# Optimization experiments

Measured on AMD Instinct MI355X. Metric: run time of the kernel, lower is better.

The kernel has to match this reference:

```python
import jax, jax.numpy as jnp
import numpy as np

THRESHOLD = 0.9
N = 20000
K = 32
F = 64


def setup_inputs() -> dict:
    key = jax.random.key(0)
    k1, k2, k3, k4, k5 = jax.random.split(key, 5)
    features = jax.random.normal(k1, (N, F), dtype=jnp.float32)
    score = jax.random.normal(k2, (N, 1), dtype=jnp.float32)
    distances = jax.random.uniform(k3, (N, K), dtype=jnp.float32)
    # two equal segments; neighbours sampled within own segment, self at col 0
    row_splits = jnp.array([0, N // 2, N], dtype=jnp.int32)
    segN = N // 2
    local_self = (jnp.arange(N, dtype=jnp.int32) % segN)
    seg_start = (jnp.arange(N, dtype=jnp.int32) // segN) * segN
    r = jax.random.randint(k4, (N, K - 1), 0, segN - 1, dtype=jnp.int32)
    r = r + (r >= local_self[:, None]).astype(jnp.int32)  # avoid sampling self
    neigh = seg_start[:, None] + r
    nidxs = jnp.concatenate([jnp.arange(N, dtype=jnp.int32)[:, None], neigh], axis=1)
    tidxs = jax.random.randint(k5, (N, 1), 0, 50, dtype=jnp.int32)
    return {"features": features, "score": score, "distances": distances,
            "nidxs": nidxs, "row_splits": row_splits, "tidxs": tidxs}


def _lnc(features, score_logits, nidxs, row_splits):
    n, k = nidxs.shape
    score = jax.nn.sigmoid(score_logits[:, 0])  # [N]
    # hierarchy order: per row-split segment, descending score
    seg_id = jnp.searchsorted(row_splits, jnp.arange(n), side='right') - 1
    order = jnp.lexsort((-score, seg_id))

    arangeK = jnp.arange(k)

    def step(carry, p):
        ggather, sel, npg, gcount = carry
        already = ggather[p] >= 0
        high = score[p] > THRESHOLD
        m = nidxs[p]                                   # [K], m[0] == p (self)
        free = (m >= 0) & (ggather[jnp.clip(m, 0, n - 1)] < 0)
        self_only = arangeK == 0
        valid = jnp.where(high, free, self_only) & (~already) & (m >= 0)
        g = gcount
        idx_w = jnp.where(valid, m, n)                 # dummy slot n for masked writes
        ggather = ggather.at[idx_w].set(g)
        row_i = jnp.where(already, n, g)
        sel = sel.at[row_i].set(jnp.where(valid, m, -1))
        npg = npg.at[row_i].set(jnp.sum(valid.astype(jnp.int32)))
        created = (~already).astype(jnp.int32)
        return (ggather, sel, npg, gcount + created), created

    init = (jnp.full((n + 1,), -1, jnp.int32),
            jnp.full((n + 1, k), -1, jnp.int32),
            jnp.zeros((n + 1,), jnp.int32),
            jnp.int32(0))
    (ggather, sel, npg, gcount), created = jax.lax.scan(step, init, order)
    ggather, sel, npg = ggather[:n], sel[:n], npg[:n]

    # new row splits: cumulative group count at segment boundaries
    cum = jnp.cumsum(created)
    rs_new = jnp.concatenate([jnp.zeros((1,), jnp.int32),
                              cum[row_splits[1:] - 1].astype(jnp.int32)])

    # pooled features per group (rows >= gcount are padding)
    sel_c = jnp.clip(sel, 0, n - 1)
    gathered = features[sel_c]                         # [N, K, F]
    mask = (sel >= 0)[..., None]
    out_mean = jnp.sum(jnp.where(mask, gathered, 0.0), axis=1)
    out_mean = out_mean / (npg[:, None].astype(features.dtype) + 1e-6)
    out_max = jnp.max(jnp.where(mask, gathered, -1000.0), axis=1)
    out = jnp.concatenate([out_mean, out_max], axis=-1)  # [N, 2F]
    backgather = ggather[:, None]
    return out, rs_new, backgather


def reference(features, score, distances, nidxs, row_splits, tidxs):
    # distances/tidxs only feed the (disabled) loss branch; kept for signature parity
    return _lnc(features, score, nidxs, row_splits)
```

## Files before the change

kernel.cpp:

```cpp
#include <hip/hip_runtime.h>


constexpr int KN = 32;
constexpr int FD = 64;
constexpr int HOCAP = 512;
constexpr int EW = 16;
constexpr int NBB = 2048;
constexpr int NT = 256;
constexpr int NMAX = 20000;
constexpr int BSLOT = 64;

typedef unsigned long long u64;


__global__ void k0_init(const float* __restrict__ score, float* __restrict__ s,
                        int* __restrict__ grab, u64* __restrict__ hlkStage,
                        int* __restrict__ hcnt, int* __restrict__ lcnt0,
                        int* __restrict__ lcnt1, u64* __restrict__ key,
                        const int* __restrict__ row_splits, int n) {
  __shared__ int ch, cl0, cl1;
  int tid = (int)threadIdx.x, bid = (int)blockIdx.x;
  int x = bid * NT + tid;
  int lane = tid & 63;
  int half = row_splits[1];
  if (tid == 0) { ch = 0; cl0 = 0; cl1 = 0; }
  __syncthreads();
  bool hi = false, lo = false;
  u64 pk = 0;
  if (x < n) {
    float sp = 1.0f / (1.0f + expf(-score[x]));
    s[x] = sp; grab[x] = 0x7FFFFFFF;
    hi = sp > 0.9f; lo = !hi;
    unsigned sb = __float_as_uint(sp);
    pk = ((u64)(x >= half) << 63) | ((u64)(0x7FFFFFFFu - sb) << 32) | (unsigned)x;
    key[x] = lo ? (((u64)sb << 32) | (u64)(0xFFFFFFFFu - (unsigned)x)) : 0ull;
  }
  u64 bh = __ballot(hi);
  u64 b0 = __ballot(lo && x < half);
  u64 b1 = __ballot(lo && x >= half);
  int base = 0;
  if (lane == 0) {
    if (bh) base = atomicAdd(&ch, __popcll(bh));
    if (b0) atomicAdd(&cl0, __popcll(b0));
    if (b1) atomicAdd(&cl1, __popcll(b1));
  }
  base = __shfl(base, 0);
  if (hi) {
    int idx = base + __popcll(bh & ((1ull << lane) - 1ull));
    if (idx < BSLOT) hlkStage[bid * BSLOT + idx] = pk;
  }
  __syncthreads();
  if (tid == 0) {
    hcnt[bid] = (ch > BSLOT) ? BSLOT : ch;
    lcnt0[bid] = cl0; lcnt1[bid] = cl1;
  }
}

__global__ __launch_bounds__(1024, 1) void kA(
    const u64* __restrict__ hlkStage, const int* __restrict__ hcnt,
    const int* __restrict__ lcnt0, const int* __restrict__ lcnt1,
    const int* __restrict__ nidxs, const int* __restrict__ row_splits,
    int* __restrict__ nbm, int* __restrict__ fgj, int* __restrict__ fgp,
    int* __restrict__ counters, int n) {
  __shared__ unsigned short hr16[NMAX];
  __shared__ unsigned E[HOCAP * EW];
  __shared__ u64 hk[HOCAP];
  __shared__ int hol[HOCAP];
  __shared__ int fgjL[HOCAP];
  __shared__ int fgpL[HOCAP];
  __shared__ int cnts[128];
  __shared__ int pref[129];
  __shared__ int lsum[2];
  __shared__ int shg;
  int tid = (int)threadIdx.x;
  int lane = tid & 63;
  int half = row_splits[1];
  int nblk = (n + NT - 1) / NT; if (nblk > 128) nblk = 128;

  {
    unsigned* h32 = (unsigned*)hr16;
    for (int i = tid; i < NMAX / 2; i += 1024) h32[i] = 0xFFFFFFFFu;
  }
  for (int i = tid; i < HOCAP * EW; i += 1024) E[i] = 0u;
  if (tid < 128) cnts[tid] = (tid < nblk) ? hcnt[tid] : 0;
  if (tid == 0) { lsum[0] = 0; lsum[1] = 0; }
  __syncthreads();

  if (tid < 64) {
    int v0 = cnts[tid], v1 = cnts[64 + tid];
#pragma unroll
    for (int off = 1; off < 64; off <<= 1) {
      int t0 = __shfl_up(v0, off), t1 = __shfl_up(v1, off);
      if (lane >= off) { v0 += t0; v1 += t1; }
    }
    int s0 = __shfl(v0, 63);
    pref[tid + 1] = v0;
    pref[64 + tid + 1] = v1 + s0;
    if (tid == 0) pref[0] = 0;
  }
  if (tid >= 64 && tid < 192) {
    int b = tid - 64;
    if (b < nblk) { atomicAdd(&lsum[0], lcnt0[b]); atomicAdd(&lsum[1], lcnt1[b]); }
  }
  __syncthreads();
  int nh = pref[nblk]; if (nh > HOCAP) nh = HOCAP;

  for (int t = tid; t < nblk * BSLOT; t += 1024) {
    int b = t >> 6, j = t & (BSLOT - 1);
    if (j < cnts[b]) {
      int d = pref[b] + j;
      if (d < HOCAP) hk[d] = hlkStage[t];
    }
  }
  __syncthreads();

  for (int i = tid; i < nh; i += 1024) {
    u64 kp = hk[i];
    int rk = 0;
#pragma unroll 8
    for (int j = 0; j < nh; ++j) rk += (hk[j] < kp) ? 1 : 0;
    int p = (int)(unsigned)(kp & 0xFFFFFFFFu);
    hol[rk] = p; hr16[p] = (unsigned short)rk;
  }
  __syncthreads();

  {
    const int4* nsrc = (const int4*)nidxs;
    int4* ndstG = (int4*)nbm;
    int tot = nh * 8;
    for (int t = tid; t < tot; t += 1024) {
      int j = t >> 3, q4 = t & 7;
      int p = hol[j];
      int4 v = nsrc[p * 8 + q4];
      ndstG[t] = v;
      unsigned bit = 1u << (j & 31);
      unsigned widx = (unsigned)(j >> 5);
      int xs[4] = { v.x, v.y, v.z, v.w };
#pragma unroll
      for (int e = 0; e < 4; ++e) {
        unsigned r = ((unsigned)xs[e] < (unsigned)n) ? hr16[xs[e]] : 0xFFFFu;
        if (r != 0xFFFFu) atomicOr(&E[r * EW + widx], bit);
      }
    }
  }
  __syncthreads();

  if (tid < 64) {
    unsigned Fw[16];
#pragma unroll
    for (int w = 0; w < 16; ++w) Fw[w] = 0u;
    int hg = 0, h0 = 0, h1 = 0;
    u64 mask_lt = (1ull << lane) - 1ull;
#pragma unroll
    for (int c = 0; c < HOCAP / 64; ++c) {
      if (c * 64 >= nh) break;
      int j = c * 64 + lane;
      bool valid = j < nh;
      unsigned er[16];
#pragma unroll
      for (int w = 0; w < 16; ++w) er[w] = valid ? E[j * EW + w] : 0u;
      unsigned acc = 0;
#pragma unroll
      for (int w = 0; w < 16; ++w) acc |= er[w] & Fw[w];
      bool base_already = acc != 0u;
      u64 erc = ((u64)er[2 * c + 1] << 32) | er[2 * c];
      u64 fb = 0;
      for (int l = 0; l < 64; ++l) {
        bool already = base_already || ((erc & fb) != 0ull);
        bool formed = valid && !already;
        fb |= __ballot(formed && (lane == l));
      }
      Fw[2 * c]     |= (unsigned)(fb & 0xFFFFFFFFull);
      Fw[2 * c + 1] |= (unsigned)(fb >> 32);
      bool formed = (fb >> lane) & 1ull;
      int p = valid ? hol[j] : 0;
      if (formed) {
        int idx = hg + __popcll(fb & mask_lt);
        fgjL[idx] = j; fgpL[idx] = p;
      }
      h0 += __popcll(__ballot(formed && p < half));
      h1 += __popcll(__ballot(formed && p >= half));
      hg += __popcll(fb);
    }
    if (lane == 0) {
      counters[1] = hg; counters[2] = h0; counters[3] = h1; shg = hg;
    }
  }
  __syncthreads();
  int hg = shg;
  for (int i = tid; i < hg; i += 1024) { fgj[i] = fgjL[i]; fgp[i] = fgpL[i]; }
  if (tid == 0) {
    counters[0] = nh;
    counters[4] = lsum[0];
    counters[5] = lsum[1];
  }
}

__global__ void kG(const float* __restrict__ s, const int* __restrict__ nbm,
                   const int* __restrict__ fgj, int* __restrict__ grab,
                   u64* __restrict__ key, int* __restrict__ counters,
                   const int* __restrict__ row_splits, int n) {
  int t = (int)(blockIdx.x * blockDim.x + threadIdx.x);
  int lane = (int)threadIdx.x & 63;
  int half = row_splits[1];
  int hg = counters[1];
  bool gl0 = false, gl1 = false;
  if (t < hg * KN) {
    int g = t >> 5;
    int x = nbm[fgj[g] * KN + (t & 31)];
    if ((unsigned)x < (unsigned)n) {
      int old = atomicMin(&grab[x], g);
      if (old == 0x7FFFFFFF && !(s[x] > 0.9f)) {
        key[x] = 0ull;
        if (x < half) gl0 = true; else gl1 = true;
      }
    }
  }
  u64 b0 = __ballot(gl0), b1 = __ballot(gl1);
  if (lane == 0) {
    if (b0) atomicSub(&counters[4], __popcll(b0));
    if (b1) atomicSub(&counters[5], __popcll(b1));
  }
}

__global__ void kB(const int* __restrict__ row_splits, const u64* __restrict__ key,
                   const int* __restrict__ grab, const int* __restrict__ nbm,
                   const int* __restrict__ fgj, const int* __restrict__ fgp,
                   const int* __restrict__ counters, int* __restrict__ gowner,
                   unsigned* __restrict__ gmask, float* __restrict__ out,
                   int n, int rs_off) {
  int tid = (int)threadIdx.x, bid = (int)blockIdx.x;
  int gtid = bid * NT + tid;
  int lane = tid & 63;
  int half = row_splits[1];
  const int GSZ = NBB * NT;
  const int NW = GSZ >> 6;
  int wid = gtid >> 6;
  int hg = counters[1], H0 = counters[2], H1 = counters[3];
  int L0 = counters[4], L1 = counters[5];
  int bg = rs_off + 3;

  for (int x = gtid; x < n; x += GSZ) {
    int prov = grab[x];
    if (prov != 0x7FFFFFFF)
      out[bg + x] = (float)((prov < H0) ? prov : (prov + L0));
  }

  for (int tsk = wid; tsk < ((n + 7) >> 3); tsk += NW) {
    int p0 = tsk * 8;
    u64 kp[8];
#pragma unroll
    for (int i = 0; i < 8; ++i) kp[i] = (p0 + i < n) ? key[p0 + i] : 0ull;
    u64 anyk = 0;
#pragma unroll
    for (int i = 0; i < 8; ++i) anyk |= kp[i];
    if (anyk == 0ull) continue;
    int base2 = (p0 < half) ? 0 : (half >> 1);
    int npair = ((p0 < half) ? half : (n - half)) >> 1;
    const ulonglong2* key2 = (const ulonglong2*)key;
    unsigned r[8] = {0, 0, 0, 0, 0, 0, 0, 0};
    for (int j = lane; j < npair; j += 64) {
      ulonglong2 kk = key2[base2 + j];
#pragma unroll
      for (int i = 0; i < 8; ++i)
        r[i] += (unsigned)((kk.x > kp[i]) + (kk.y > kp[i]));
    }
#pragma unroll
    for (int i = 0; i < 8; ++i) {
#pragma unroll
      for (int off = 32; off > 0; off >>= 1) r[i] += __shfl_down(r[i], off);
    }
    if (lane == 0) {
#pragma unroll
      for (int i = 0; i < 8; ++i) {
        if (kp[i] == 0ull) continue;
        int p = p0 + i;
        int base = (p < half) ? H0 : (H0 + L0 + H1);
        int gid = base + (int)r[i];
        gowner[gid] = p; gmask[gid] = 1u;
        out[bg + p] = (float)gid;
      }
    }
  }

  for (int t = gtid; t < hg * KN; t += GSZ) {
    int g = t >> 5, k = t & 31;
    int x = nbm[fgj[g] * KN + k];
    u64 b = __ballot(grab[x] == g);
    if (k == 0) {
      unsigned w = (lane >= 32) ? (unsigned)(b >> 32) : (unsigned)b;
      int gid2 = (g < H0) ? g : (g + L0);
      gowner[gid2] = fgp[g]; gmask[gid2] = w;
    }
  }

  if (gtid == 0) {
    out[rs_off + 0] = 0.0f;
    out[rs_off + 1] = (float)(H0 + L0);
    out[rs_off + 2] = (float)(H0 + L0 + H1 + L1);
  }
}

__global__ void kC(const float* __restrict__ feat, const int* __restrict__ nidxs,
                   const int* __restrict__ gowner, const unsigned* __restrict__ gmask,
                   const int* __restrict__ counters, float* __restrict__ out, int n) {
  int gtid = (int)(blockIdx.x * blockDim.x + threadIdx.x);
  int wid = gtid >> 6;
  int f = gtid & 63;
  const int NW = (NBB * NT) >> 6;
  int G = counters[2] + counters[3] + counters[4] + counters[5];
  for (int row = wid; row < n; row += NW) {
    float mean, mx;
    if (row < G) {
      int owner = gowner[row];
      unsigned mask = gmask[row];
      int npg = __popc(mask);
      float sum = 0.0f; mx = -1000.0f;
      for (int k = 0; k < KN; ++k) {
        if (mask & (1u << k)) {
          int m = nidxs[owner * KN + k];
          float v = feat[m * FD + f];
          sum += v; mx = fmaxf(mx, v);
        }
      }
      mean = sum / ((float)npg + 1e-6f);
    } else {
      mean = 0.0f; mx = -1000.0f;
    }
    out[row * (2 * FD) + f] = mean;
    out[row * (2 * FD) + FD + f] = mx;
  }
}

extern "C" void kernel_launch(void* const* d_in, const int* in_sizes, int n_in,
                              void* d_out, int out_size, void* d_ws, size_t ws_size,
                              hipStream_t stream) {
  const float* features   = (const float*)d_in[0];
  const float* score      = (const float*)d_in[1];
  const int*   nidxs      = (const int*)d_in[3];
  const int*   row_splits = (const int*)d_in[4];
  int n = in_sizes[1];
  float* out = (float*)d_out;
  int* wsi = (int*)d_ws;
  int rs_off = n * 2 * FD;

  int*      counters = wsi;
  float*    s        = (float*)(wsi + 8);
  int*      grab     = wsi + 8 + n;
  u64*      key      = (u64*)(wsi + 8 + 2 * n);
  int*      gowner   = wsi + 8 + 4 * n;
  int*      nbm      = wsi + 8 + 5 * n;
  int*      fgj      = wsi + 8 + 5 * n + HOCAP * KN;
  int*      fgp      = fgj + HOCAP;
  u64*      hlkStage = (u64*)(fgp + HOCAP);
  int*      hcnt     = (int*)(hlkStage + 128 * BSLOT);
  int*      lcnt0    = hcnt + 128;
  int*      lcnt1    = lcnt0 + 128;
  unsigned* gmask    = (unsigned*)s;

  int blocks = (n + NT - 1) / NT;
  k0_init<<<blocks, NT, 0, stream>>>(score, s, grab, hlkStage, hcnt, lcnt0,
                                     lcnt1, key, row_splits, n);
  kA<<<1, 1024, 0, stream>>>(hlkStage, hcnt, lcnt0, lcnt1, nidxs, row_splits,
                             nbm, fgj, fgp, counters, n);
  kG<<<(HOCAP * KN) / NT, NT, 0, stream>>>(s, nbm, fgj, grab, key, counters,
                                           row_splits, n);
  kB<<<NBB, NT, 0, stream>>>(row_splits, key, grab, nbm, fgj, fgp, counters,
                             gowner, gmask, out, n, rs_off);
  kC<<<NBB, NT, 0, stream>>>(features, nidxs, gowner, gmask, counters, out, n);
}
```

Baseline: 85.30 us.

## Fuse group assignment and feature pooling into one kernel, dropping owner/mask buffers

New measurement: 74.32 us. 1.15x faster.

```diff
diff --git a/kernel.cpp b/kernel.cpp
--- a/kernel.cpp
+++ b/kernel.cpp
@@ -60,14 +60,13 @@
     const u64* __restrict__ hlkStage, const int* __restrict__ hcnt,
     const int* __restrict__ lcnt0, const int* __restrict__ lcnt1,
     const int* __restrict__ nidxs, const int* __restrict__ row_splits,
-    int* __restrict__ nbm, int* __restrict__ fgj, int* __restrict__ fgp,
-    int* __restrict__ counters, int n) {
+    int* __restrict__ nbm, int* __restrict__ fgj, int* __restrict__ counters,
+    int n) {
   __shared__ unsigned short hr16[NMAX];
   __shared__ unsigned E[HOCAP * EW];
   __shared__ u64 hk[HOCAP];
   __shared__ int hol[HOCAP];
   __shared__ int fgjL[HOCAP];
-  __shared__ int fgpL[HOCAP];
   __shared__ int cnts[128];
   __shared__ int pref[129];
   __shared__ int lsum[2];
@@ -176,7 +175,7 @@
       int p = valid ? hol[j] : 0;
       if (formed) {
         int idx = hg + __popcll(fb & mask_lt);
-        fgjL[idx] = j; fgpL[idx] = p;
+        fgjL[idx] = j;
       }
       h0 += __popcll(__ballot(formed && p < half));
       h1 += __popcll(__ballot(formed && p >= half));
@@ -188,7 +187,7 @@
   }
   __syncthreads();
   int hg = shg;
-  for (int i = tid; i < hg; i += 1024) { fgj[i] = fgjL[i]; fgp[i] = fgpL[i]; }
+  for (int i = tid; i < hg; i += 1024) fgj[i] = fgjL[i];
   if (tid == 0) {
     counters[0] = nh;
     counters[4] = lsum[0];
@@ -223,12 +222,11 @@
   }
 }
 
-__global__ void kB(const int* __restrict__ row_splits, const u64* __restrict__ key,
-                   const int* __restrict__ grab, const int* __restrict__ nbm,
-                   const int* __restrict__ fgj, const int* __restrict__ fgp,
-                   const int* __restrict__ counters, int* __restrict__ gowner,
-                   unsigned* __restrict__ gmask, float* __restrict__ out,
-                   int n, int rs_off) {
+__global__ void kBC(const int* __restrict__ row_splits, const u64* __restrict__ key,
+                    const int* __restrict__ grab, const int* __restrict__ nbm,
+                    const int* __restrict__ fgj, const int* __restrict__ counters,
+                    const float* __restrict__ feat, float* __restrict__ out,
+                    int n, int rs_off) {
   int tid = (int)threadIdx.x, bid = (int)blockIdx.x;
   int gtid = bid * NT + tid;
   int lane = tid & 63;
@@ -238,7 +236,9 @@
   int wid = gtid >> 6;
   int hg = counters[1], H0 = counters[2], H1 = counters[3];
   int L0 = counters[4], L1 = counters[5];
+  int G = H0 + H1 + L0 + L1;
   int bg = rs_off + 3;
+  const float inv1 = 1.0f / (1.0f + 1e-6f);
 
   for (int x = gtid; x < n; x += GSZ) {
     int prov = grab[x];
@@ -246,89 +246,79 @@
       out[bg + x] = (float)((prov < H0) ? prov : (prov + L0));
   }
 
-  for (int tsk = wid; tsk < ((n + 7) >> 3); tsk += NW) {
-    int p0 = tsk * 8;
-    u64 kp[8];
-#pragma unroll
-    for (int i = 0; i < 8; ++i) kp[i] = (p0 + i < n) ? key[p0 + i] : 0ull;
-    u64 anyk = 0;
-#pragma unroll
-    for (int i = 0; i < 8; ++i) anyk |= kp[i];
-    if (anyk == 0ull) continue;
+  for (int row = G + wid; row < n; row += NW) {
+    out[row * (2 * FD) + lane] = 0.0f;
+    out[row * (2 * FD) + FD + lane] = -1000.0f;
+  }
+
+  for (int tsk = wid; tsk < ((n + 3) >> 2); tsk += NW) {
+    int p0 = tsk * 4;
+    u64 kp0 = key[p0];
+    u64 kp1 = (p0 + 1 < n) ? key[p0 + 1] : 0ull;
+    u64 kp2 = (p0 + 2 < n) ? key[p0 + 2] : 0ull;
+    u64 kp3 = (p0 + 3 < n) ? key[p0 + 3] : 0ull;
+    if ((kp0 | kp1 | kp2 | kp3) == 0ull) continue;
     int base2 = (p0 < half) ? 0 : (half >> 1);
     int npair = ((p0 < half) ? half : (n - half)) >> 1;
     const ulonglong2* key2 = (const ulonglong2*)key;
-    unsigned r[8] = {0, 0, 0, 0, 0, 0, 0, 0};
+    unsigned r0 = 0, r1 = 0, r2 = 0, r3 = 0;
     for (int j = lane; j < npair; j += 64) {
       ulonglong2 kk = key2[base2 + j];
-#pragma unroll
-      for (int i = 0; i < 8; ++i)
-        r[i] += (unsigned)((kk.x > kp[i]) + (kk.y > kp[i]));
-    }
-#pragma unroll
-    for (int i = 0; i < 8; ++i) {
-#pragma unroll
-      for (int off = 32; off > 0; off >>= 1) r[i] += __shfl_down(r[i], off);
-    }
-    if (lane == 0) {
-#pragma unroll
-      for (int i = 0; i < 8; ++i) {
-        if (kp[i] == 0ull) continue;
-        int p = p0 + i;
-        int base = (p < half) ? H0 : (H0 + L0 + H1);
-        int gid = base + (int)r[i];
-        gowner[gid] = p; gmask[gid] = 1u;
-        out[bg + p] = (float)gid;
-      }
-    }
-  }
-
-  for (int t = gtid; t < hg * KN; t += GSZ) {
-    int g = t >> 5, k = t & 31;
-    int x = nbm[fgj[g] * KN + k];
-    u64 b = __ballot(grab[x] == g);
-    if (k == 0) {
-      unsigned w = (lane >= 32) ? (unsigned)(b >> 32) : (unsigned)b;
-      int gid2 = (g < H0) ? g : (g + L0);
-      gowner[gid2] = fgp[g]; gmask[gid2] = w;
-    }
+      r0 += (unsigned)((kk.x > kp0) + (kk.y > kp0));
+      r1 += (unsigned)((kk.x > kp1) + (kk.y > kp1));
+      r2 += (unsigned)((kk.x > kp2) + (kk.y > kp2));
+      r3 += (unsigned)((kk.x > kp3) + (kk.y > kp3));
+    }
+#pragma unroll
+    for (int off = 32; off > 0; off >>= 1) {
+      r0 += __shfl_down(r0, off);
+      r1 += __shfl_down(r1, off);
+      r2 += __shfl_down(r2, off);
+      r3 += __shfl_down(r3, off);
+    }
+    r0 = __shfl(r0, 0); r1 = __shfl(r1, 0); r2 = __shfl(r2, 0); r3 = __shfl(r3, 0);
+    unsigned rr[4] = { r0, r1, r2, r3 };
+    u64 kps[4] = { kp0, kp1, kp2, kp3 };
+#pragma unroll
+    for (int j = 0; j < 4; ++j) {
+      if (kps[j] == 0ull) continue;
+      int p = p0 + j;
+      int base = (p < half) ? H0 : (H0 + L0 + H1);
+      int gid = base + (int)rr[j];
+      float v = feat[p * FD + lane];
+      out[gid * (2 * FD) + lane] = v * inv1;
+      out[gid * (2 * FD) + FD + lane] = v;
+      if (lane == 0) out[bg + p] = (float)gid;
+    }
+  }
+
+  for (int g = wid; g < hg; g += NW) {
+    int x = 0;
+    bool mine = false;
+    if (lane < KN) {
+      x = nbm[fgj[g] * KN + lane];
+      mine = (grab[x] == g);
+    }
+    u64 bal = __ballot(mine);
+    unsigned mask = (unsigned)(bal & 0xFFFFFFFFull);
+    int npg = __popc(mask);
+    float sum = 0.0f, mx = -1000.0f;
+    for (int k = 0; k < KN; ++k) {
+      if (mask & (1u << k)) {
+        int m = __shfl(x, k);
+        float v = feat[m * FD + lane];
+        sum += v; mx = fmaxf(mx, v);
+      }
+    }
+    int gid2 = (g < H0) ? g : (g + L0);
+    out[gid2 * (2 * FD) + lane] = sum / ((float)npg + 1e-6f);
+    out[gid2 * (2 * FD) + FD + lane] = mx;
   }
 
   if (gtid == 0) {
     out[rs_off + 0] = 0.0f;
     out[rs_off + 1] = (float)(H0 + L0);
     out[rs_off + 2] = (float)(H0 + L0 + H1 + L1);
-  }
-}
-
-__global__ void kC(const float* __restrict__ feat, const int* __restrict__ nidxs,
-                   const int* __restrict__ gowner, const unsigned* __restrict__ gmask,
-                   const int* __restrict__ counters, float* __restrict__ out, int n) {
-  int gtid = (int)(blockIdx.x * blockDim.x + threadIdx.x);
-  int wid = gtid >> 6;
-  int f = gtid & 63;
-  const int NW = (NBB * NT) >> 6;
-  int G = counters[2] + counters[3] + counters[4] + counters[5];
-  for (int row = wid; row < n; row += NW) {
-    float mean, mx;
-    if (row < G) {
-      int owner = gowner[row];
-      unsigned mask = gmask[row];
-      int npg = __popc(mask);
-      float sum = 0.0f; mx = -1000.0f;
-      for (int k = 0; k < KN; ++k) {
-        if (mask & (1u << k)) {
-          int m = nidxs[owner * KN + k];
-          float v = feat[m * FD + f];
-          sum += v; mx = fmaxf(mx, v);
-        }
-      }
-      mean = sum / ((float)npg + 1e-6f);
-    } else {
-      mean = 0.0f; mx = -1000.0f;
-    }
-    out[row * (2 * FD) + f] = mean;
-    out[row * (2 * FD) + FD + f] = mx;
   }
 }
 
@@ -348,24 +338,20 @@
   float*    s        = (float*)(wsi + 8);
   int*      grab     = wsi + 8 + n;
   u64*      key      = (u64*)(wsi + 8 + 2 * n);
-  int*      gowner   = wsi + 8 + 4 * n;
   int*      nbm      = wsi + 8 + 5 * n;
   int*      fgj      = wsi + 8 + 5 * n + HOCAP * KN;
-  int*      fgp      = fgj + HOCAP;
-  u64*      hlkStage = (u64*)(fgp + HOCAP);
+  u64*      hlkStage = (u64*)(fgj + 2 * HOCAP);
   int*      hcnt     = (int*)(hlkStage + 128 * BSLOT);
   int*      lcnt0    = hcnt + 128;
   int*      lcnt1    = lcnt0 + 128;
-  unsigned* gmask    = (unsigned*)s;
 
   int blocks = (n + NT - 1) / NT;
   k0_init<<<blocks, NT, 0, stream>>>(score, s, grab, hlkStage, hcnt, lcnt0,
                                      lcnt1, key, row_splits, n);
   kA<<<1, 1024, 0, stream>>>(hlkStage, hcnt, lcnt0, lcnt1, nidxs, row_splits,
-                             nbm, fgj, fgp, counters, n);
+                             nbm, fgj, counters, n);
   kG<<<(HOCAP * KN) / NT, NT, 0, stream>>>(s, nbm, fgj, grab, key, counters,
                                            row_splits, n);
-  kB<<<NBB, NT, 0, stream>>>(row_splits, key, grab, nbm, fgj, fgp, counters,
-                             gowner, gmask, out, n, rs_off);
-  kC<<<NBB, NT, 0, stream>>>(features, nidxs, gowner, gmask, counters, out, n);
-}
+  kBC<<<NBB, NT, 0, stream>>>(row_splits, key, grab, nbm, fgj, counters,
+                              features, out, n, rs_off);
+}
```
